# Performance work log

Measured on AMD Instinct MI355X. Metric: run time of the kernel, lower is better.

Reference implementation:

```python
import jax, jax.numpy as jnp
import numpy as np

NUM_USERS = 100000
NUM_ITEMS = 50000
EMB = 64
N_LAYERS = 3
NNZ = 4800000
N_NODES = NUM_USERS + NUM_ITEMS


def setup_inputs() -> dict:
    key = jax.random.key(0)
    k1, k2, k3, k4, k5 = jax.random.split(key, 5)
    emb_user = jax.random.normal(k1, (NUM_USERS, EMB), dtype=jnp.float32) * 0.1
    emb_item = jax.random.normal(k2, (NUM_ITEMS, EMB), dtype=jnp.float32) * 0.1
    adj_rows = jax.random.randint(k3, (NNZ,), 0, N_NODES, dtype=jnp.int32)
    adj_cols = jax.random.randint(k4, (NNZ,), 0, N_NODES, dtype=jnp.int32)
    # normalized adjacency values (stand-in for D^-1/2 A D^-1/2 entries)
    adj_vals = jax.random.uniform(k5, (NNZ,), dtype=jnp.float32) / 32.0
    return {
        "emb_user": emb_user,
        "emb_item": emb_item,
        "adj_vals": adj_vals,
        "adj_rows": adj_rows,
        "adj_cols": adj_cols,
    }


def _spmm(vals, rows, cols, x):
    # y[r] = sum_{e: rows[e]==r} vals[e] * x[cols[e]]
    gathered = x[cols] * vals[:, None]  # [nnz, emb]
    return jax.ops.segment_sum(gathered, rows, num_segments=N_NODES)


def reference(emb_user, emb_item, adj_vals, adj_rows, adj_cols):
    ego = jnp.concatenate([emb_user, emb_item], axis=0)  # [(U+I), emb]
    acc = ego
    h = ego
    for _ in range(N_LAYERS):
        h = _spmm(adj_vals, adj_rows, adj_cols, h)
        acc = acc + h
    mean_emb = acc / jnp.float32(N_LAYERS + 1)
    user_embeddings = mean_emb[:NUM_USERS]
    item_embeddings = mean_emb[NUM_USERS:]
    return user_embeddings, item_embeddings
```

## Files before the change

### kernel.cpp

```cpp
#include <hip/hip_runtime.h>
#include <hip/hip_bf16.h>

#define N_USERS   100000
#define N_ITEMS   50000
#define N_NODES_C 150000
#define EMB       64
#define N_ELEM    (N_NODES_C * EMB)
#define BKT_SHIFT 9
#define NBKT      ((N_NODES_C + 511) >> 9)
#define BKT_CAP   20480
#define CH_EDGES  4096
#define EPT       16

typedef unsigned int u32x4 __attribute__((ext_vector_type(4)));
typedef unsigned int u32x2 __attribute__((ext_vector_type(2)));
typedef unsigned long long u64;

__device__ __forceinline__ unsigned int bf16_bits(float f) {
    __hip_bfloat16 h = __float2bfloat16(f);
    return (unsigned int)reinterpret_cast<unsigned short&>(h);
}
__device__ __forceinline__ float lo_bf(unsigned int u) {
    return __uint_as_float(u << 16);
}
__device__ __forceinline__ float hi_bf(unsigned int u) {
    return __uint_as_float(u & 0xFFFF0000u);
}

__device__ __forceinline__ int probe_emb_bf16(const void* eu, int lane) {
    unsigned w = ((const unsigned*)eu)[lane];
    unsigned e = (w >> 7) & 0xFFu;
    return __popcll(__ballot(e >= 100u && e <= 127u)) > 32;
}
__device__ __forceinline__ int probe_vals_bf16(const void* vals, int lane) {
    unsigned w = ((const unsigned*)vals)[lane];
    return __popcll(__ballot((w >> 15) & 1u)) < 8;
}

__global__ void prep_fused(const int* __restrict__ rows, const int* __restrict__ cols,
                           const void* __restrict__ vals,
                           u64* __restrict__ tmp, int* __restrict__ tails, int nnz,
                           int nchunks,
                           const void* __restrict__ eu, const void* __restrict__ ei,
                           __hip_bfloat16* __restrict__ h0) {
    int t = threadIdx.x;
    int lane = t & 63;
    if ((int)blockIdx.x >= nchunks) {
        int ebf = probe_emb_bf16(eu, lane);
        int q = ((int)blockIdx.x - nchunks) * 256 + t;
        if (q >= (N_ELEM >> 2)) return;
        const int uquads = (N_USERS * EMB) >> 2;
        u32x2 o;
        if (ebf) {
            o = (q < uquads) ? *((const u32x2*)eu + q)
                             : *((const u32x2*)ei + (q - uquads));
        } else {
            const uint4 f = (q < uquads) ? *((const uint4*)eu + q)
                                         : *((const uint4*)ei + (q - uquads));
            unsigned r0, r1;
            asm("v_cvt_pk_bf16_f32 %0, %1, %2" : "=v"(r0)
                : "v"(__uint_as_float(f.x)), "v"(__uint_as_float(f.y)));
            asm("v_cvt_pk_bf16_f32 %0, %1, %2" : "=v"(r1)
                : "v"(__uint_as_float(f.z)), "v"(__uint_as_float(f.w)));
            o.x = r0; o.y = r1;
        }
        *reinterpret_cast<u32x2*>(h0 + ((size_t)q << 2)) = o;
        return;
    }
    __shared__ int lcnt[NBKT];
    __shared__ int lbase[NBKT];
    int vbf = probe_vals_bf16(vals, lane);
    for (int b = t; b < NBKT; b += 256) lcnt[b] = 0;
    __syncthreads();
    int base = blockIdx.x * CH_EDGES;
    u64 pk[EPT];
    unsigned int br[EPT];
    #pragma unroll
    for (int i = 0; i < EPT; ++i) {
        int e = base + i * 256 + t;
        if (e < nnz) {
            int r = rows[e];
            int c = cols[e];
            float v = vbf ? __bfloat162float(((const __hip_bfloat16*)vals)[e])
                          : ((const float*)vals)[e];
            int bk = r >> BKT_SHIFT;
            int rk = atomicAdd(&lcnt[bk], 1);
            pk[i] = ((u64)(unsigned)r << 34)
                  | ((u64)(unsigned)c << 16)
                  | (u64)bf16_bits(v);
            br[i] = ((unsigned)bk << 16) | (unsigned)rk;
        } else {
            br[i] = 0xFFFFFFFFu;
        }
    }
    __syncthreads();
    for (int b = t; b < NBKT; b += 256)
        lbase[b] = lcnt[b] ? atomicAdd(&tails[b], lcnt[b]) : 0;
    __syncthreads();
    #pragma unroll
    for (int i = 0; i < EPT; ++i) {
        if (br[i] != 0xFFFFFFFFu) {
            int bk = br[i] >> 16, rk = br[i] & 0xFFFFu;
            int pos = lbase[bk] + rk;
            if (pos < BKT_CAP)
                tmp[(size_t)bk * BKT_CAP + pos] = pk[i];
        }
    }
}

__global__ void bucket_csr(const u64* __restrict__ tmp,
                           int2* __restrict__ edges,
                           const int* __restrict__ tails,
                           int* __restrict__ row_ptr) {
    __shared__ int cnt[512];
    __shared__ int off[512];
    __shared__ int wsum[8];
    int b = blockIdx.x, t = threadIdx.x;
    int lane = t & 63, wid = t >> 6;
    int rowbase = b << BKT_SHIFT;
    int nrows = N_NODES_C - rowbase; if (nrows > 512) nrows = 512;
    int n = tails[b]; if (n > BKT_CAP) n = BKT_CAP;
    const u64* src = tmp + (size_t)b * BKT_CAP;
    int pre = 0;
    for (int i = t; i < b; i += 512) {
        int v = tails[i];
        pre += (v > BKT_CAP) ? BKT_CAP : v;
    }
    #pragma unroll
    for (int m = 1; m < 64; m <<= 1) pre += __shfl_xor(pre, m, 64);
    cnt[t] = 0;
    if (lane == 0) wsum[wid] = pre;
    __syncthreads();
    int obase = 0;
    #pragma unroll
    for (int i = 0; i < 8; ++i) obase += wsum[i];
    for (int e = t; e < n; e += 512)
        atomicAdd(&cnt[(int)(src[e] >> 34) - rowbase], 1);
    __syncthreads();
    int v = cnt[t];
    int sc = v;
    #pragma unroll
    for (int m = 1; m < 64; m <<= 1) {
        int u = __shfl_up(sc, m, 64);
        if (lane >= m) sc += u;
    }
    if (lane == 63) wsum[wid] = sc;
    __syncthreads();
    int woff = 0;
    for (int i = 0; i < wid; ++i) woff += wsum[i];
    int excl = obase + woff + sc - v;
    off[t] = excl;
    if (t < nrows) row_ptr[rowbase + t] = excl;
    if (b == NBKT - 1 && t == 0) row_ptr[N_NODES_C] = obase + n;
    __syncthreads();
    for (int e = t; e < n; e += 512) {
        u64 p = src[e];
        int rloc = (int)(p >> 34) - rowbase;
        unsigned c = (unsigned)((p >> 16) & 0x3FFFFu);
        int pos = atomicAdd(&off[rloc], 1);
        edges[pos] = make_int2((int)(c << 7), (int)((unsigned)(p & 0xFFFFu) << 16));
    }
}

#define DOT2Q(wA, wB, vp, ae, ao)                                              \
    {                                                                          \
        unsigned _xe = __builtin_amdgcn_perm((wA), (wB), 0x01000504u);         \
        unsigned _xo = __builtin_amdgcn_perm((wA), (wB), 0x03020706u);         \
        asm("v_dot2_f32_bf16 %0, %1, %2, %0" : "+v"(ae) : "v"(_xe), "v"(vp));  \
        asm("v_dot2_f32_bf16 %0, %1, %2, %0" : "+v"(ao) : "v"(_xo), "v"(vp));  \
    }

#define SWZ_ADD(a, pat) \
    a += __int_as_float(__builtin_amdgcn_ds_swizzle(__float_as_int(a), pat))

__global__ void spmm8(const __hip_bfloat16* __restrict__ x,
                      __hip_bfloat16* __restrict__ y,
                      const u64* __restrict__ edges,
                      const int* __restrict__ row_ptr,
                      const __hip_bfloat16* __restrict__ h0,
                      const __hip_bfloat16* __restrict__ h1,
                      void* __restrict__ out,
                      const void* __restrict__ eu,
                      int last) {
    int lane = threadIdx.x & 63;
    int ebf = 0;
    if (last) ebf = probe_emb_bf16(eu, lane);
    int row = __builtin_amdgcn_readfirstlane(blockIdx.x * 4 + (threadIdx.x >> 6));
    if (row >= N_NODES_C) return;
    int slot = lane >> 3;
    int s    = lane & 7;
    int beg = row_ptr[row], end = row_ptr[row + 1];
    const char* xb = (const char*)x;
    const char* eb = (const char*)edges;
    unsigned s16 = (unsigned)s << 4;
    unsigned eoff = ((unsigned)(beg + slot)) << 3;
    float a0 = 0.f, a1 = 0.f, a2 = 0.f, a3 = 0.f,
          a4 = 0.f, a5 = 0.f, a6 = 0.f, a7 = 0.f;
    for (int e = beg; e < end; e += 32, eoff += 256) {
        int rem = end - e;
        const u64* ep = (const u64*)(eb + eoff);
        u64 pA = (slot      < rem) ? __builtin_nontemporal_load(ep)      : 0ULL;
        u64 pB = (slot + 8  < rem) ? __builtin_nontemporal_load(ep + 8)  : 0ULL;
        u64 pC = (slot + 16 < rem) ? __builtin_nontemporal_load(ep + 16) : 0ULL;
        u64 pD = (slot + 24 < rem) ? __builtin_nontemporal_load(ep + 24) : 0ULL;
        unsigned oA = (unsigned)pA + s16;
        unsigned oB = (unsigned)pB + s16;
        unsigned oC = (unsigned)pC + s16;
        unsigned oD = (unsigned)pD + s16;
        const uint4 gA = *reinterpret_cast<const uint4*>(xb + oA);
        const uint4 gB = *reinterpret_cast<const uint4*>(xb + oB);
        const uint4 gC = *reinterpret_cast<const uint4*>(xb + oC);
        const uint4 gD = *reinterpret_cast<const uint4*>(xb + oD);
        unsigned vAB = __builtin_amdgcn_perm((unsigned)(pA >> 32),
                                             (unsigned)(pB >> 32), 0x03020706u);
        unsigned vCD = __builtin_amdgcn_perm((unsigned)(pC >> 32),
                                             (unsigned)(pD >> 32), 0x03020706u);
        DOT2Q(gA.x, gB.x, vAB, a0, a1);
        DOT2Q(gA.y, gB.y, vAB, a2, a3);
        DOT2Q(gA.z, gB.z, vAB, a4, a5);
        DOT2Q(gA.w, gB.w, vAB, a6, a7);
        DOT2Q(gC.x, gD.x, vCD, a0, a1);
        DOT2Q(gC.y, gD.y, vCD, a2, a3);
        DOT2Q(gC.z, gD.z, vCD, a4, a5);
        DOT2Q(gC.w, gD.w, vCD, a6, a7);
    }
    SWZ_ADD(a0, 0x201F); SWZ_ADD(a1, 0x201F); SWZ_ADD(a2, 0x201F); SWZ_ADD(a3, 0x201F);
    SWZ_ADD(a4, 0x201F); SWZ_ADD(a5, 0x201F); SWZ_ADD(a6, 0x201F); SWZ_ADD(a7, 0x201F);
    SWZ_ADD(a0, 0x401F); SWZ_ADD(a1, 0x401F); SWZ_ADD(a2, 0x401F); SWZ_ADD(a3, 0x401F);
    SWZ_ADD(a4, 0x401F); SWZ_ADD(a5, 0x401F); SWZ_ADD(a6, 0x401F); SWZ_ADD(a7, 0x401F);
    a0 += __shfl_xor(a0, 32, 64);
    a1 += __shfl_xor(a1, 32, 64);
    a2 += __shfl_xor(a2, 32, 64);
    a3 += __shfl_xor(a3, 32, 64);
    a4 += __shfl_xor(a4, 32, 64);
    a5 += __shfl_xor(a5, 32, 64);
    a6 += __shfl_xor(a6, 32, 64);
    a7 += __shfl_xor(a7, 32, 64);
    if (slot != 0) return;
    size_t base = ((size_t)row << 6) + (s << 3);
    if (!last) {
        unsigned q0, q1, q2, q3;
        asm("v_cvt_pk_bf16_f32 %0, %1, %2" : "=v"(q0) : "v"(a0), "v"(a1));
        asm("v_cvt_pk_bf16_f32 %0, %1, %2" : "=v"(q1) : "v"(a2), "v"(a3));
        asm("v_cvt_pk_bf16_f32 %0, %1, %2" : "=v"(q2) : "v"(a4), "v"(a5));
        asm("v_cvt_pk_bf16_f32 %0, %1, %2" : "=v"(q3) : "v"(a6), "v"(a7));
        u32x4 o; o.x = q0; o.y = q1; o.z = q2; o.w = q3;
        *reinterpret_cast<u32x4*>(y + base) = o;
    } else {
        const uint4 r0 = *reinterpret_cast<const uint4*>(h0 + base);
        const uint4 r1 = *reinterpret_cast<const uint4*>(h1 + base);
        const uint4 r2 = *reinterpret_cast<const uint4*>(x + base);
        float f0 = (lo_bf(r0.x) + lo_bf(r1.x) + lo_bf(r2.x) + a0) * 0.25f;
        float f1 = (hi_bf(r0.x) + hi_bf(r1.x) + hi_bf(r2.x) + a1) * 0.25f;
        float f2 = (lo_bf(r0.y) + lo_bf(r1.y) + lo_bf(r2.y) + a2) * 0.25f;
        float f3 = (hi_bf(r0.y) + hi_bf(r1.y) + hi_bf(r2.y) + a3) * 0.25f;
        float f4 = (lo_bf(r0.z) + lo_bf(r1.z) + lo_bf(r2.z) + a4) * 0.25f;
        float f5 = (hi_bf(r0.z) + hi_bf(r1.z) + hi_bf(r2.z) + a5) * 0.25f;
        float f6 = (lo_bf(r0.w) + lo_bf(r1.w) + lo_bf(r2.w) + a6) * 0.25f;
        float f7 = (hi_bf(r0.w) + hi_bf(r1.w) + hi_bf(r2.w) + a7) * 0.25f;
        if (ebf) {
            unsigned q0, q1, q2, q3;
            asm("v_cvt_pk_bf16_f32 %0, %1, %2" : "=v"(q0) : "v"(f0), "v"(f1));
            asm("v_cvt_pk_bf16_f32 %0, %1, %2" : "=v"(q1) : "v"(f2), "v"(f3));
            asm("v_cvt_pk_bf16_f32 %0, %1, %2" : "=v"(q2) : "v"(f4), "v"(f5));
            asm("v_cvt_pk_bf16_f32 %0, %1, %2" : "=v"(q3) : "v"(f6), "v"(f7));
            u32x4 o; o.x = q0; o.y = q1; o.z = q2; o.w = q3;
            __builtin_nontemporal_store(
                o, reinterpret_cast<u32x4*>((__hip_bfloat16*)out + base));
        } else {
            float* op = (float*)out + base;
            u32x4 q0, q1;
            q0.x = __float_as_uint(f0); q0.y = __float_as_uint(f1);
            q0.z = __float_as_uint(f2); q0.w = __float_as_uint(f3);
            q1.x = __float_as_uint(f4); q1.y = __float_as_uint(f5);
            q1.z = __float_as_uint(f6); q1.w = __float_as_uint(f7);
            __builtin_nontemporal_store(q0, reinterpret_cast<u32x4*>(op));
            __builtin_nontemporal_store(q1, reinterpret_cast<u32x4*>(op + 4));
        }
    }
}

extern "C" void kernel_launch(void* const* d_in, const int* in_sizes, int n_in,
                              void* d_out, int out_size, void* d_ws, size_t ws_size,
                              hipStream_t stream) {
    const void* eu   = d_in[0];
    const void* ei   = d_in[1];
    const void* vals = d_in[2];
    const int*  rows = (const int*)d_in[3];
    const int*  cols = (const int*)d_in[4];
    const int nnz = in_sizes[2];

    __hip_bfloat16* h[3];
    h[0] = (__hip_bfloat16*)d_ws;
    h[1] = h[0] + N_ELEM;
    h[2] = h[1] + N_ELEM;
    int2* edges   = (int2*)(h[2] + N_ELEM);
    int* row_ptr  = (int*)(edges + nnz);
    int* tails    = row_ptr + (N_NODES_C + 1);
    char* pt = (char*)(tails + NBKT);
    u64* tmp = (u64*)(((uintptr_t)pt + 7) & ~(uintptr_t)7);

    hipMemsetAsync(tails, 0, NBKT * sizeof(int), stream);

    int nchunks = (nnz + CH_EDGES - 1) / CH_EDGES;
    int ninit = ((N_ELEM >> 2) + 255) / 256;
    prep_fused<<<nchunks + ninit, 256, 0, stream>>>(rows, cols, vals, tmp, tails,
                                                    nnz, nchunks, eu, ei, h[0]);
    bucket_csr<<<NBKT, 512, 0, stream>>>(tmp, edges, tails, row_ptr);

    int nsb = (N_NODES_C + 3) / 4;
    spmm8<<<nsb, 256, 0, stream>>>(h[0], h[1], (const u64*)edges, row_ptr,
                                   nullptr, nullptr, nullptr, eu, 0);
    spmm8<<<nsb, 256, 0, stream>>>(h[1], h[2], (const u64*)edges, row_ptr,
                                   nullptr, nullptr, nullptr, eu, 0);
    spmm8<<<nsb, 256, 0, stream>>>(h[2], nullptr, (const u64*)edges, row_ptr,
                                   h[0], h[1], d_out, eu, 1);
}
```

Before: 501.7 us.

## Stage bucketed edges in shared memory for coalesced scatter, halve bucket size

In prep_fused, each chunk's packed edge records are first sorted by bucket into shared memory using a local prefix scan of bucket counts. They are then written to the global bucket arrays in contiguous runs, replacing per-edge scattered stores. Buckets are halved to 256 rows, which gives more bucket_csr blocks of 256 threads and smaller per-block shared arrays. This adds 32KB of LDS per prep block, which may reduce occupancy, plus an extra scan and sync phase.

```diff
diff --git a/kernel.cpp b/kernel.cpp
--- a/kernel.cpp
+++ b/kernel.cpp
@@ -6,9 +6,9 @@
 #define N_NODES_C 150000
 #define EMB       64
 #define N_ELEM    (N_NODES_C * EMB)
-#define BKT_SHIFT 9
-#define NBKT      ((N_NODES_C + 511) >> 9)
-#define BKT_CAP   20480
+#define BKT_SHIFT 8
+#define NBKT      ((N_NODES_C + 255) >> 8)
+#define BKT_CAP   10240
 #define CH_EDGES  4096
 #define EPT       16
 
@@ -43,8 +43,13 @@
                            int nchunks,
                            const void* __restrict__ eu, const void* __restrict__ ei,
                            __hip_bfloat16* __restrict__ h0) {
+    __shared__ u64 srec[CH_EDGES];
+    __shared__ int lcnt[NBKT];
+    __shared__ int lofs[NBKT];
+    __shared__ int gbase[NBKT];
+    __shared__ int wsum[4];
     int t = threadIdx.x;
-    int lane = t & 63;
+    int lane = t & 63, wid = t >> 6;
     if ((int)blockIdx.x >= nchunks) {
         int ebf = probe_emb_bf16(eu, lane);
         int q = ((int)blockIdx.x - nchunks) * 256 + t;
@@ -67,12 +72,11 @@
         *reinterpret_cast<u32x2*>(h0 + ((size_t)q << 2)) = o;
         return;
     }
-    __shared__ int lcnt[NBKT];
-    __shared__ int lbase[NBKT];
     int vbf = probe_vals_bf16(vals, lane);
     for (int b = t; b < NBKT; b += 256) lcnt[b] = 0;
     __syncthreads();
     int base = blockIdx.x * CH_EDGES;
+    int nvalid = nnz - base; if (nvalid > CH_EDGES) nvalid = CH_EDGES;
     u64 pk[EPT];
     unsigned int br[EPT];
     #pragma unroll
@@ -94,17 +98,44 @@
         }
     }
     __syncthreads();
-    for (int b = t; b < NBKT; b += 256)
-        lbase[b] = lcnt[b] ? atomicAdd(&tails[b], lcnt[b]) : 0;
+    {
+        int i0 = 3 * t;
+        int c0 = (i0     < NBKT) ? lcnt[i0]     : 0;
+        int c1 = (i0 + 1 < NBKT) ? lcnt[i0 + 1] : 0;
+        int c2 = (i0 + 2 < NBKT) ? lcnt[i0 + 2] : 0;
+        int csum = c0 + c1 + c2;
+        int sc = csum;
+        #pragma unroll
+        for (int m = 1; m < 64; m <<= 1) {
+            int u = __shfl_up(sc, m, 64);
+            if (lane >= m) sc += u;
+        }
+        if (lane == 63) wsum[wid] = sc;
+        __syncthreads();
+        int woff = 0;
+        for (int i = 0; i < wid; ++i) woff += wsum[i];
+        int ex = woff + sc - csum;
+        if (i0     < NBKT) lofs[i0]     = ex;
+        if (i0 + 1 < NBKT) lofs[i0 + 1] = ex + c0;
+        if (i0 + 2 < NBKT) lofs[i0 + 2] = ex + c0 + c1;
+    }
     __syncthreads();
     #pragma unroll
     for (int i = 0; i < EPT; ++i) {
         if (br[i] != 0xFFFFFFFFu) {
             int bk = br[i] >> 16, rk = br[i] & 0xFFFFu;
-            int pos = lbase[bk] + rk;
-            if (pos < BKT_CAP)
-                tmp[(size_t)bk * BKT_CAP + pos] = pk[i];
-        }
+            srec[lofs[bk] + rk] = pk[i];
+        }
+    }
+    for (int b = t; b < NBKT; b += 256)
+        gbase[b] = lcnt[b] ? atomicAdd(&tails[b], lcnt[b]) : 0;
+    __syncthreads();
+    for (int j = t; j < nvalid; j += 256) {
+        u64 rec = srec[j];
+        int bk = (int)(rec >> 42);
+        int gpos = gbase[bk] + (j - lofs[bk]);
+        if (gpos < BKT_CAP)
+            tmp[(size_t)bk * BKT_CAP + gpos] = rec;
     }
 }
 
@@ -112,17 +143,17 @@
                            int2* __restrict__ edges,
                            const int* __restrict__ tails,
                            int* __restrict__ row_ptr) {
-    __shared__ int cnt[512];
-    __shared__ int off[512];
-    __shared__ int wsum[8];
+    __shared__ int cnt[256];
+    __shared__ int off[256];
+    __shared__ int wsum[4];
     int b = blockIdx.x, t = threadIdx.x;
     int lane = t & 63, wid = t >> 6;
     int rowbase = b << BKT_SHIFT;
-    int nrows = N_NODES_C - rowbase; if (nrows > 512) nrows = 512;
+    int nrows = N_NODES_C - rowbase; if (nrows > 256) nrows = 256;
     int n = tails[b]; if (n > BKT_CAP) n = BKT_CAP;
     const u64* src = tmp + (size_t)b * BKT_CAP;
     int pre = 0;
-    for (int i = t; i < b; i += 512) {
+    for (int i = t; i < b; i += 256) {
         int v = tails[i];
         pre += (v > BKT_CAP) ? BKT_CAP : v;
     }
@@ -131,10 +162,8 @@
     cnt[t] = 0;
     if (lane == 0) wsum[wid] = pre;
     __syncthreads();
-    int obase = 0;
-    #pragma unroll
-    for (int i = 0; i < 8; ++i) obase += wsum[i];
-    for (int e = t; e < n; e += 512)
+    int obase = wsum[0] + wsum[1] + wsum[2] + wsum[3];
+    for (int e = t; e < n; e += 256)
         atomicAdd(&cnt[(int)(src[e] >> 34) - rowbase], 1);
     __syncthreads();
     int v = cnt[t];
@@ -153,7 +182,7 @@
     if (t < nrows) row_ptr[rowbase + t] = excl;
     if (b == NBKT - 1 && t == 0) row_ptr[N_NODES_C] = obase + n;
     __syncthreads();
-    for (int e = t; e < n; e += 512) {
+    for (int e = t; e < n; e += 256) {
         u64 p = src[e];
         int rloc = (int)(p >> 34) - rowbase;
         unsigned c = (unsigned)((p >> 16) & 0x3FFFFu);
@@ -306,7 +335,7 @@
     int ninit = ((N_ELEM >> 2) + 255) / 256;
     prep_fused<<<nchunks + ninit, 256, 0, stream>>>(rows, cols, vals, tmp, tails,
                                                     nnz, nchunks, eu, ei, h[0]);
-    bucket_csr<<<NBKT, 512, 0, stream>>>(tmp, edges, tails, row_ptr);
+    bucket_csr<<<NBKT, 256, 0, stream>>>(tmp, edges, tails, row_ptr);
 
     int nsb = (N_NODES_C + 3) / 4;
     spmm8<<<nsb, 256, 0, stream>>>(h[0], h[1], (const u64*)edges, row_ptr,
```

After: 504.9 us. No clear change (+0.6%).

## Replace bucketed two-pass CSR build with global histogram, scan, atomic scatter

Applied to the files above, without the earlier changes.

Replaces the bucket-based CSR construction (local bucket counts, a temp buffer, then a per-bucket sort) with three kernels: a global per-row atomic histogram fused with the embedding init, a per-block prefix scan into row_ptr and cursor, and a scatter that takes one global atomic per edge. It removes the 8-byte-per-edge temp buffer round trip and the fixed bucket capacity limit. In exchange, rows and cols are read twice and every edge does a global atomic with scattered writes. Edge order within a row becomes nondeterministic, and build_rowptr re-sums all previous counts in each block.

```diff
diff --git a/kernel.cpp b/kernel.cpp
--- a/kernel.cpp
+++ b/kernel.cpp
@@ -6,11 +6,8 @@
 #define N_NODES_C 150000
 #define EMB       64
 #define N_ELEM    (N_NODES_C * EMB)
-#define BKT_SHIFT 9
-#define NBKT      ((N_NODES_C + 511) >> 9)
-#define BKT_CAP   20480
-#define CH_EDGES  4096
-#define EPT       16
+#define NBKT      ((N_NODES_C + 255) >> 8)
+#define EPT_E     8
 
 typedef unsigned int u32x4 __attribute__((ext_vector_type(4)));
 typedef unsigned int u32x2 __attribute__((ext_vector_type(2)));
@@ -37,17 +34,14 @@
     return __popcll(__ballot((w >> 15) & 1u)) < 8;
 }
 
-__global__ void prep_fused(const int* __restrict__ rows, const int* __restrict__ cols,
-                           const void* __restrict__ vals,
-                           u64* __restrict__ tmp, int* __restrict__ tails, int nnz,
-                           int nchunks,
-                           const void* __restrict__ eu, const void* __restrict__ ei,
-                           __hip_bfloat16* __restrict__ h0) {
-    int t = threadIdx.x;
-    int lane = t & 63;
-    if ((int)blockIdx.x >= nchunks) {
+__global__ void hist_init(const int* __restrict__ rows,
+                          int* __restrict__ row_cnt, int nnz, int nhist,
+                          const void* __restrict__ eu, const void* __restrict__ ei,
+                          __hip_bfloat16* __restrict__ h0) {
+    int t = threadIdx.x, lane = t & 63;
+    if ((int)blockIdx.x >= nhist) {
         int ebf = probe_emb_bf16(eu, lane);
-        int q = ((int)blockIdx.x - nchunks) * 256 + t;
+        int q = ((int)blockIdx.x - nhist) * 256 + t;
         if (q >= (N_ELEM >> 2)) return;
         const int uquads = (N_USERS * EMB) >> 2;
         u32x2 o;
@@ -67,98 +61,64 @@
         *reinterpret_cast<u32x2*>(h0 + ((size_t)q << 2)) = o;
         return;
     }
-    __shared__ int lcnt[NBKT];
-    __shared__ int lbase[NBKT];
+    int base = blockIdx.x * (EPT_E * 256);
+    #pragma unroll
+    for (int i = 0; i < EPT_E; ++i) {
+        int e = base + i * 256 + t;
+        if (e < nnz) atomicAdd(&row_cnt[rows[e]], 1);
+    }
+}
+
+__global__ void build_rowptr(const int* __restrict__ row_cnt,
+                             int* __restrict__ row_ptr,
+                             int* __restrict__ cursor) {
+    __shared__ int wsum[4];
+    int b = blockIdx.x, t = threadIdx.x;
+    int lane = t & 63, wid = t >> 6;
+    int rbase = b << 8;
+    int pre = 0;
+    for (int i = t; i < rbase; i += 256) pre += row_cnt[i];
+    #pragma unroll
+    for (int m = 1; m < 64; m <<= 1) pre += __shfl_xor(pre, m, 64);
+    if (lane == 0) wsum[wid] = pre;
+    __syncthreads();
+    int obase = wsum[0] + wsum[1] + wsum[2] + wsum[3];
+    __syncthreads();
+    int r = rbase + t;
+    int cnt = (r < N_NODES_C) ? row_cnt[r] : 0;
+    int sc = cnt;
+    #pragma unroll
+    for (int m = 1; m < 64; m <<= 1) {
+        int u = __shfl_up(sc, m, 64);
+        if (lane >= m) sc += u;
+    }
+    if (lane == 63) wsum[wid] = sc;
+    __syncthreads();
+    int woff = 0;
+    for (int i = 0; i < wid; ++i) woff += wsum[i];
+    int excl = obase + woff + sc - cnt;
+    if (r < N_NODES_C) { row_ptr[r] = excl; cursor[r] = excl; }
+    if (b == NBKT - 1 && t == 255) row_ptr[N_NODES_C] = excl + cnt;
+}
+
+__global__ void scatter_csr(const int* __restrict__ rows, const int* __restrict__ cols,
+                            const void* __restrict__ vals,
+                            int* __restrict__ cursor, int2* __restrict__ edges,
+                            int nnz) {
+    int t = threadIdx.x, lane = t & 63;
     int vbf = probe_vals_bf16(vals, lane);
-    for (int b = t; b < NBKT; b += 256) lcnt[b] = 0;
-    __syncthreads();
-    int base = blockIdx.x * CH_EDGES;
-    u64 pk[EPT];
-    unsigned int br[EPT];
-    #pragma unroll
-    for (int i = 0; i < EPT; ++i) {
+    int base = blockIdx.x * (EPT_E * 256);
+    #pragma unroll
+    for (int i = 0; i < EPT_E; ++i) {
         int e = base + i * 256 + t;
         if (e < nnz) {
             int r = rows[e];
             int c = cols[e];
             float v = vbf ? __bfloat162float(((const __hip_bfloat16*)vals)[e])
                           : ((const float*)vals)[e];
-            int bk = r >> BKT_SHIFT;
-            int rk = atomicAdd(&lcnt[bk], 1);
-            pk[i] = ((u64)(unsigned)r << 34)
-                  | ((u64)(unsigned)c << 16)
-                  | (u64)bf16_bits(v);
-            br[i] = ((unsigned)bk << 16) | (unsigned)rk;
-        } else {
-            br[i] = 0xFFFFFFFFu;
+            int pos = atomicAdd(&cursor[r], 1);
+            edges[pos] = make_int2(c << 7, (int)(bf16_bits(v) << 16));
         }
-    }
-    __syncthreads();
-    for (int b = t; b < NBKT; b += 256)
-        lbase[b] = lcnt[b] ? atomicAdd(&tails[b], lcnt[b]) : 0;
-    __syncthreads();
-    #pragma unroll
-    for (int i = 0; i < EPT; ++i) {
-        if (br[i] != 0xFFFFFFFFu) {
-            int bk = br[i] >> 16, rk = br[i] & 0xFFFFu;
-            int pos = lbase[bk] + rk;
-            if (pos < BKT_CAP)
-                tmp[(size_t)bk * BKT_CAP + pos] = pk[i];
-        }
-    }
-}
-
-__global__ void bucket_csr(const u64* __restrict__ tmp,
-                           int2* __restrict__ edges,
-                           const int* __restrict__ tails,
-                           int* __restrict__ row_ptr) {
-    __shared__ int cnt[512];
-    __shared__ int off[512];
-    __shared__ int wsum[8];
-    int b = blockIdx.x, t = threadIdx.x;
-    int lane = t & 63, wid = t >> 6;
-    int rowbase = b << BKT_SHIFT;
-    int nrows = N_NODES_C - rowbase; if (nrows > 512) nrows = 512;
-    int n = tails[b]; if (n > BKT_CAP) n = BKT_CAP;
-    const u64* src = tmp + (size_t)b * BKT_CAP;
-    int pre = 0;
-    for (int i = t; i < b; i += 512) {
-        int v = tails[i];
-        pre += (v > BKT_CAP) ? BKT_CAP : v;
-    }
-    #pragma unroll
-    for (int m = 1; m < 64; m <<= 1) pre += __shfl_xor(pre, m, 64);
-    cnt[t] = 0;
-    if (lane == 0) wsum[wid] = pre;
-    __syncthreads();
-    int obase = 0;
-    #pragma unroll
-    for (int i = 0; i < 8; ++i) obase += wsum[i];
-    for (int e = t; e < n; e += 512)
-        atomicAdd(&cnt[(int)(src[e] >> 34) - rowbase], 1);
-    __syncthreads();
-    int v = cnt[t];
-    int sc = v;
-    #pragma unroll
-    for (int m = 1; m < 64; m <<= 1) {
-        int u = __shfl_up(sc, m, 64);
-        if (lane >= m) sc += u;
-    }
-    if (lane == 63) wsum[wid] = sc;
-    __syncthreads();
-    int woff = 0;
-    for (int i = 0; i < wid; ++i) woff += wsum[i];
-    int excl = obase + woff + sc - v;
-    off[t] = excl;
-    if (t < nrows) row_ptr[rowbase + t] = excl;
-    if (b == NBKT - 1 && t == 0) row_ptr[N_NODES_C] = obase + n;
-    __syncthreads();
-    for (int e = t; e < n; e += 512) {
-        u64 p = src[e];
-        int rloc = (int)(p >> 34) - rowbase;
-        unsigned c = (unsigned)((p >> 16) & 0x3FFFFu);
-        int pos = atomicAdd(&off[rloc], 1);
-        edges[pos] = make_int2((int)(c << 7), (int)((unsigned)(p & 0xFFFFu) << 16));
     }
 }
 
@@ -296,17 +256,17 @@
     h[2] = h[1] + N_ELEM;
     int2* edges   = (int2*)(h[2] + N_ELEM);
     int* row_ptr  = (int*)(edges + nnz);
-    int* tails    = row_ptr + (N_NODES_C + 1);
-    char* pt = (char*)(tails + NBKT);
-    u64* tmp = (u64*)(((uintptr_t)pt + 7) & ~(uintptr_t)7);
-
-    hipMemsetAsync(tails, 0, NBKT * sizeof(int), stream);
-
-    int nchunks = (nnz + CH_EDGES - 1) / CH_EDGES;
+    int* row_cnt  = row_ptr + (N_NODES_C + 1);
+    int* cursor   = row_cnt + N_NODES_C;
+
+    hipMemsetAsync(row_cnt, 0, N_NODES_C * sizeof(int), stream);
+
+    int nhist = (nnz + EPT_E * 256 - 1) / (EPT_E * 256);
     int ninit = ((N_ELEM >> 2) + 255) / 256;
-    prep_fused<<<nchunks + ninit, 256, 0, stream>>>(rows, cols, vals, tmp, tails,
-                                                    nnz, nchunks, eu, ei, h[0]);
-    bucket_csr<<<NBKT, 512, 0, stream>>>(tmp, edges, tails, row_ptr);
+    hist_init<<<nhist + ninit, 256, 0, stream>>>(rows, row_cnt, nnz, nhist,
+                                                 eu, ei, h[0]);
+    build_rowptr<<<NBKT, 256, 0, stream>>>(row_cnt, row_ptr, cursor);
+    scatter_csr<<<nhist, 256, 0, stream>>>(rows, cols, vals, cursor, edges, nnz);
 
     int nsb = (N_NODES_C + 3) / 4;
     spmm8<<<nsb, 256, 0, stream>>>(h[0], h[1], (const u64*)edges, row_ptr,
```

After: 893.7 us. +78.1%, slower.
